# Kernel optimization log

Hardware: AMD Instinct MI355X
Metric: run time of the kernel (lower is better)

## Reference

```python
import jax, jax.numpy as jnp
import numpy as np

B, S, HID = 4, 2048, 2048
NH, NKV, HD = 16, 4, 128  # head_dim = HID // NH
Q_SIZE, KV_SIZE = NH * HD, NKV * HD


def setup_inputs() -> dict:
    key = jax.random.key(0)
    ks = jax.random.split(key, 8)
    pos = jnp.arange(S, dtype=jnp.float32)[:, None]
    inv_freq = 1.0 / (10000.0 ** (jnp.arange(0, HD, 2, dtype=jnp.float32) / HD))  # [HD/2]
    ang = pos * inv_freq[None, :]  # [S, HD/2]
    return {
        "hidden_states": jax.random.normal(ks[0], (B, S, HID), jnp.float32),
        "rotary_pos_emb_cos": jnp.cos(ang),
        "rotary_pos_emb_sin": jnp.sin(ang),
        "w_qkv": jax.random.normal(ks[1], (HID, Q_SIZE + 2 * KV_SIZE), jnp.float32) * (HID ** -0.5),
        "b_qkv": jax.random.normal(ks[2], (Q_SIZE + 2 * KV_SIZE,), jnp.float32) * 0.02,
        "w_o": jax.random.normal(ks[3], (HID, HID), jnp.float32) * (HID ** -0.5),
        "b_o": jax.random.normal(ks[4], (HID,), jnp.float32) * 0.02,
    }


def _apply_rope(x, cos, sin):
    # x: [B, S, H, D]; cos/sin: [S, D/2]; rotate-half (non-interleaved) convention
    d2 = x.shape[-1] // 2
    x1, x2 = x[..., :d2], x[..., d2:]
    c = cos[None, :, None, :]
    s = sin[None, :, None, :]
    return jnp.concatenate([x1 * c - x2 * s, x2 * c + x1 * s], axis=-1)


def reference(hidden_states, rotary_pos_emb_cos, rotary_pos_emb_sin, w_qkv, b_qkv, w_o, b_o):
    b, s, _ = hidden_states.shape
    qkv = hidden_states @ w_qkv + b_qkv  # [B, S, Q_SIZE + 2*KV_SIZE]
    q, k, v = jnp.split(qkv, [Q_SIZE, Q_SIZE + KV_SIZE], axis=-1)
    q = q.reshape(b, s, NH, HD)
    k = k.reshape(b, s, NKV, HD)
    v = v.reshape(b, s, NKV, HD)
    q = _apply_rope(q, rotary_pos_emb_cos, rotary_pos_emb_sin)
    k = _apply_rope(k, rotary_pos_emb_cos, rotary_pos_emb_sin)
    # grouped-query attention: repeat kv heads to match query heads
    g = NH // NKV
    k = jnp.repeat(k, g, axis=2)  # [B, S, NH, HD]
    v = jnp.repeat(v, g, axis=2)
    scale = HD ** -0.5
    scores = jnp.einsum("bshd,bthd->bhst", q, k) * scale  # [B, NH, S, S]
    probs = jax.nn.softmax(scores, axis=-1)
    out = jnp.einsum("bhst,bthd->bshd", probs, v)  # [B, S, NH, HD]
    out = out.reshape(b, s, NH * HD)
    return out @ w_o + b_o
```

## Files before the change

### kernel.cpp

```cpp
#include <hip/hip_runtime.h>
#include <math.h>

#define B_N   4
#define S_N   2048
#define HID_N 2048
#define NH_N  16
#define NKV_N 4
#define HD_N  128
#define QSZ   2048
#define KVSZ  512
#define QKVN  3072
#define M_N   8192

typedef __bf16 bf16;
typedef __bf16 bf16x8 __attribute__((ext_vector_type(8)));
typedef float  f32x4  __attribute__((ext_vector_type(4)));

#define GLL16(gp, lp)                                                          \
  __builtin_amdgcn_global_load_lds(                                            \
      (const __attribute__((address_space(1))) void*)(gp),                     \
      (__attribute__((address_space(3))) void*)(lp), 16, 0, 0)

__device__ __forceinline__ f32x4 mfma16(bf16x8 a, bf16x8 b, f32x4 c) {
  return __builtin_amdgcn_mfma_f32_16x16x32_bf16(a, b, c, 0, 0, 0);
}

__global__ __launch_bounds__(256) void conv_bf16_kernel(
    const float* __restrict__ X, bf16* __restrict__ Y)
{
  size_t i = ((size_t)blockIdx.x * 256 + threadIdx.x) * 8;
  float4 a = *(const float4*)&X[i];
  float4 b = *(const float4*)&X[i + 4];
  union { bf16 h[8]; uint4 u; } pk;
  pk.h[0] = (bf16)a.x; pk.h[1] = (bf16)a.y; pk.h[2] = (bf16)a.z; pk.h[3] = (bf16)a.w;
  pk.h[4] = (bf16)b.x; pk.h[5] = (bf16)b.y; pk.h[6] = (bf16)b.z; pk.h[7] = (bf16)b.w;
  *(uint4*)&Y[i] = pk.u;
}

__global__ __launch_bounds__(256) void convT_kernel(
    const float* __restrict__ W, bf16* __restrict__ Wt, int K, int N)
{
  __shared__ __attribute__((aligned(16))) bf16 tile[64 * 68];
  const int n0 = blockIdx.x * 64, k0 = blockIdx.y * 64;
#pragma unroll
  for (int it = 0; it < 4; ++it) {
    int idx = it * 256 + threadIdx.x;
    int r = idx >> 4, c4 = (idx & 15) << 2;
    float4 v = *(const float4*)&W[(size_t)(k0 + r) * N + n0 + c4];
    union { bf16 h[4]; unsigned long long u; } pk;
    pk.h[0] = (bf16)v.x; pk.h[1] = (bf16)v.y; pk.h[2] = (bf16)v.z; pk.h[3] = (bf16)v.w;
    *(unsigned long long*)&tile[r * 68 + c4] = pk.u;
  }
  __syncthreads();
#pragma unroll
  for (int it = 0; it < 4; ++it) {
    int idx = it * 256 + threadIdx.x;
    int rn = idx >> 4, ck4 = (idx & 15) << 2;
    union { bf16 h[4]; unsigned long long u; } pk;
#pragma unroll
    for (int i = 0; i < 4; ++i) pk.h[i] = tile[(ck4 + i) * 68 + rn];
    *(unsigned long long*)&Wt[(size_t)(n0 + rn) * K + k0 + ck4] = pk.u;
  }
}

template <bool OUT_BF16>
__global__ __launch_bounds__(256, 2) void gemm_bf16_kernel(
    const bf16* __restrict__ A, const bf16* __restrict__ Bt,
    const float* __restrict__ bias, void* __restrict__ Cout,
    int M, int N, int K)
{
  __shared__ __attribute__((aligned(16))) bf16 As[2][128 * 32];
  __shared__ __attribute__((aligned(16))) bf16 Bs[2][128 * 32];

  const int tid  = threadIdx.x;
  const int lane = tid & 63, wv = tid >> 6;
  const int quad = lane >> 4, ln = lane & 15;
  const int row0 = blockIdx.y * 128, col0 = blockIdx.x * 128;
  const int wr = (wv >> 1) * 64, wc = (wv & 1) * 64;

  f32x4 acc[4][4];
  const f32x4 zero = {0.f, 0.f, 0.f, 0.f};
#pragma unroll
  for (int mt = 0; mt < 4; ++mt)
#pragma unroll
    for (int nt = 0; nt < 4; ++nt) acc[mt][nt] = zero;

  const int s0 = wv * 128 + lane;
  const bf16* gA0 = A  + (size_t)(row0 + (s0 >> 2)) * K + (s0 & 3) * 8;
  const bf16* gA1 = gA0 + 16 * (size_t)K;
  const bf16* gB0 = Bt + (size_t)(col0 + (s0 >> 2)) * K + (s0 & 3) * 8;
  const bf16* gB1 = gB0 + 16 * (size_t)K;
  const int lofs0 = wv * 1024, lofs1 = lofs0 + 512;

  GLL16(gA0, &As[0][lofs0]);
  GLL16(gA1, &As[0][lofs1]);
  GLL16(gB0, &Bs[0][lofs0]);
  GLL16(gB1, &Bs[0][lofs1]);
  __syncthreads();

  int cur = 0;
  for (int k0 = 0; k0 < K; k0 += 32, cur ^= 1) {
    const int nk = k0 + 32;
    if (nk < K) {
      GLL16(gA0 + nk, &As[cur ^ 1][lofs0]);
      GLL16(gA1 + nk, &As[cur ^ 1][lofs1]);
      GLL16(gB0 + nk, &Bs[cur ^ 1][lofs0]);
      GLL16(gB1 + nk, &Bs[cur ^ 1][lofs1]);
    }

    bf16x8 a[4], b[4];
#pragma unroll
    for (int mt = 0; mt < 4; ++mt)
      a[mt] = *(const bf16x8*)&As[cur][(wr + mt * 16 + ln) * 32 + quad * 8];
#pragma unroll
    for (int nt = 0; nt < 4; ++nt)
      b[nt] = *(const bf16x8*)&Bs[cur][(wc + nt * 16 + ln) * 32 + quad * 8];
#pragma unroll
    for (int mt = 0; mt < 4; ++mt)
#pragma unroll
      for (int nt = 0; nt < 4; ++nt)
        acc[mt][nt] = mfma16(a[mt], b[nt], acc[mt][nt]);

    __syncthreads();
  }

#pragma unroll
  for (int nt = 0; nt < 4; ++nt) {
    const int c = col0 + wc + nt * 16 + ln;
    const float bv = bias[c];
#pragma unroll
    for (int mt = 0; mt < 4; ++mt) {
#pragma unroll
      for (int r = 0; r < 4; ++r) {
        const int rr = row0 + wr + mt * 16 + quad * 4 + r;
        const float v = acc[mt][nt][r] + bv;
        if (OUT_BF16) ((bf16*)Cout)[(size_t)rr * N + c] = (bf16)v;
        else          ((float*)Cout)[(size_t)rr * N + c] = v;
      }
    }
  }
}

__global__ __launch_bounds__(256) void rope_repack_kernel(
    const bf16* __restrict__ qkvB, const float* __restrict__ cosb,
    const float* __restrict__ sinb, bf16* __restrict__ Qb, bf16* __restrict__ Kb)
{
  int idx = blockIdx.x * 256 + threadIdx.x;
  int j  = idx & 63;
  int m  = (idx >> 6) & (M_N - 1);
  int hh = idx >> 19;
  int b = m >> 11, s = m & (S_N - 1);
  float c  = cosb[s * 64 + j];
  float sn = sinb[s * 64 + j];
  if (hh < NH_N) {
    const bf16* src = qkvB + (size_t)m * QKVN + hh * HD_N;
    float x1 = (float)src[j], x2 = (float)src[j + 64];
    bf16* dst = Qb + ((size_t)(b * NH_N + hh) * S_N + s) * HD_N;
    const float qs = 0.08838834764831845f * 1.4426950408889634f;
    dst[j]      = (bf16)((x1 * c - x2 * sn) * qs);
    dst[j + 64] = (bf16)((x2 * c + x1 * sn) * qs);
  } else {
    int kh = hh - NH_N;
    const bf16* src = qkvB + (size_t)m * QKVN + QSZ + kh * HD_N;
    float x1 = (float)src[j], x2 = (float)src[j + 64];
    bf16* dst = Kb + ((size_t)(b * NKV_N + kh) * S_N + s) * HD_N;
    dst[j]      = (bf16)(x1 * c - x2 * sn);
    dst[j + 64] = (bf16)(x2 * c + x1 * sn);
  }
}

__global__ __launch_bounds__(256) void transposeV_kernel(
    const bf16* __restrict__ qkvB, bf16* __restrict__ Vt)
{
  __shared__ __attribute__((aligned(16))) bf16 tile[64 * 136];
  const int s0 = blockIdx.x * 64;
  const int bkh = blockIdx.y;
  const int b = bkh >> 2, kh = bkh & 3;
#pragma unroll
  for (int it = 0; it < 4; ++it) {
    int ci = it * 256 + threadIdx.x;
    int r = ci >> 4, c = ci & 15;
    uint4 v = *(const uint4*)&qkvB[(size_t)(b * S_N + s0 + r) * QKVN +
                                   QSZ + KVSZ + kh * HD_N + c * 8];
    *(uint4*)&tile[r * 136 + c * 8] = v;
  }
  __syncthreads();
#pragma unroll
  for (int it = 0; it < 4; ++it) {
    int ci = it * 256 + threadIdx.x;
    int d = ci >> 3, c = ci & 7;
    union { bf16 h[8]; uint4 u; } pk;
#pragma unroll
    for (int i = 0; i < 8; ++i) pk.h[i] = tile[(c * 8 + i) * 136 + d];
    *(uint4*)&Vt[((size_t)bkh * HD_N + d) * S_N + s0 + c * 8] = pk.u;
  }
}

__global__ __launch_bounds__(256, 3) void attn_mfma_kernel(
    const bf16* __restrict__ Qb, const bf16* __restrict__ Kb,
    const bf16* __restrict__ Vt, bf16* __restrict__ Ob)
{
  __shared__ __attribute__((aligned(16))) bf16 Ks[2][32 * 128];
  __shared__ __attribute__((aligned(16))) bf16 Vs[2][128 * 32];
  __shared__ __attribute__((aligned(16))) bf16 Ps[128 * 40];

  const int tid  = threadIdx.x;
  const int lane = tid & 63, wv = tid >> 6;
  const int quad = lane >> 4, ln = lane & 15;

  const int gid = blockIdx.x;
  const int xcd = gid & 7, sl = gid >> 3;
  const int grp = xcd * 2 + (sl >> 6);
  const int within = sl & 63;
  const int b = grp >> 2, kh = grp & 3;
  const int h = kh * 4 + (within >> 4);
  const int q0 = (within & 15) * 128;

  const bf16* Qg = Qb + ((size_t)(b * NH_N + h) * S_N + q0) * HD_N;
  const bf16* Kg = Kb + (size_t)(b * NKV_N + kh) * S_N * HD_N;
  const bf16* Vg = Vt + (size_t)(b * NKV_N + kh) * HD_N * S_N;

  bf16x8 aq[2][4];
#pragma unroll
  for (int g = 0; g < 2; ++g) {
    const bf16* qrow = Qg + (size_t)((wv * 2 + g) * 16 + ln) * HD_N;
#pragma unroll
    for (int dc = 0; dc < 4; ++dc)
      aq[g][dc] = *(const bf16x8*)&qrow[(dc * 4 + quad) * 8];
  }

  const bf16* kga[2];
  const bf16* vga[2];
#pragma unroll
  for (int t = 0; t < 2; ++t) {
    int slot = (t * 4 + wv) * 64 + lane;
    int row = slot >> 4, cc = slot & 15;
    int csrc = (cc & 8) | ((cc & 7) ^ (row & 7));
    kga[t] = Kg + (size_t)row * 128 + csrc * 8;
    int dv = slot >> 2, ccv = slot & 3;
    int csv = ccv ^ ((dv >> 1) & 3);
    vga[t] = Vg + (size_t)dv * S_N + csv * 8;
  }

#pragma unroll
  for (int t = 0; t < 2; ++t) GLL16(kga[t], &Ks[0][(t * 4 + wv) * 512]);
#pragma unroll
  for (int t = 0; t < 2; ++t) GLL16(vga[t], &Vs[0][(t * 4 + wv) * 512]);

  bf16x8 bones;
#pragma unroll
  for (int j = 0; j < 8; ++j) bones[j] = (ln == 0) ? (bf16)1.0f : (bf16)0.0f;

  f32x4 accO[2][8];
  const f32x4 zero = {0.f, 0.f, 0.f, 0.f};
#pragma unroll
  for (int g = 0; g < 2; ++g)
#pragma unroll
    for (int dt = 0; dt < 8; ++dt) accO[g][dt] = zero;
  f32x4 accL[2] = {zero, zero};

  __syncthreads();

  int cur = 0;
  for (int kt = 0; kt < S_N; kt += 32, cur ^= 1) {
    const int nkt = kt + 32;
    if (nkt < S_N) {
#pragma unroll
      for (int t = 0; t < 2; ++t)
        GLL16(kga[t] + (size_t)nkt * 128, &Ks[cur ^ 1][(t * 4 + wv) * 512]);
#pragma unroll
      for (int t = 0; t < 2; ++t)
        GLL16(vga[t] + nkt, &Vs[cur ^ 1][(t * 4 + wv) * 512]);
    }
    const bf16* Kc = Ks[cur];
    const bf16* Vc = Vs[cur];

    f32x4 accS[2][2];
#pragma unroll
    for (int g = 0; g < 2; ++g)
#pragma unroll
      for (int nt = 0; nt < 2; ++nt) accS[g][nt] = zero;
#pragma unroll
    for (int nt = 0; nt < 2; ++nt) {
      const int kp = nt * 16 + ln;
#pragma unroll
      for (int dc = 0; dc < 4; ++dc) {
        int c = dc * 4 + quad;
        int cs = (c & 8) | ((c & 7) ^ (kp & 7));
        bf16x8 bk = *(const bf16x8*)&Kc[kp * 128 + cs * 8];
        accS[0][nt] = mfma16(aq[0][dc], bk, accS[0][nt]);
        accS[1][nt] = mfma16(aq[1][dc], bk, accS[1][nt]);
      }
    }

#pragma unroll
    for (int g = 0; g < 2; ++g)
#pragma unroll
      for (int r = 0; r < 4; ++r) {
        const int q = (wv * 2 + g) * 16 + quad * 4 + r;
        bf16* pr = &Ps[q * 40 + ln];
        pr[0]  = (bf16)__builtin_amdgcn_exp2f(accS[g][0][r]);
        pr[16] = (bf16)__builtin_amdgcn_exp2f(accS[g][1][r]);
      }

    bf16x8 ap[2];
#pragma unroll
    for (int g = 0; g < 2; ++g) {
      ap[g] = *(const bf16x8*)&Ps[((wv * 2 + g) * 16 + ln) * 40 + quad * 8];
      accL[g] = mfma16(ap[g], bones, accL[g]);
    }
#pragma unroll
    for (int dt = 0; dt < 8; ++dt) {
      const int d = dt * 16 + ln;
      int cs = quad ^ ((d >> 1) & 3);
      bf16x8 bv = *(const bf16x8*)&Vc[d * 32 + cs * 8];
      accO[0][dt] = mfma16(ap[0], bv, accO[0][dt]);
      accO[1][dt] = mfma16(ap[1], bv, accO[1][dt]);
    }

    __syncthreads();
  }

#pragma unroll
  for (int g = 0; g < 2; ++g)
#pragma unroll
    for (int r = 0; r < 4; ++r) {
      const float l = __shfl(accL[g][r], lane & 48);
      const float inv = 1.f / l;
      const int q = q0 + (wv * 2 + g) * 16 + quad * 4 + r;
      const size_t base = ((size_t)b * S_N + q) * HID_N + h * HD_N;
#pragma unroll
      for (int dt = 0; dt < 8; ++dt)
        Ob[base + dt * 16 + ln] = (bf16)(accO[g][dt][r] * inv);
    }
}

extern "C" void kernel_launch(void* const* d_in, const int* in_sizes, int n_in,
                              void* d_out, int out_size, void* d_ws, size_t ws_size,
                              hipStream_t stream) {
  const float* hidden = (const float*)d_in[0];
  const float* cosb   = (const float*)d_in[1];
  const float* sinb   = (const float*)d_in[2];
  const float* w_qkv  = (const float*)d_in[3];
  const float* b_qkv  = (const float*)d_in[4];
  const float* w_o    = (const float*)d_in[5];
  const float* b_o    = (const float*)d_in[6];
  float* out = (float*)d_out;

  char* w = (char*)d_ws;
  bf16* qkvB  = (bf16*)(w);
  bf16* Qb    = (bf16*)(w + 50331648);
  bf16* Kb    = (bf16*)(w + 83886080);
  bf16* Vt    = (bf16*)(w + 92274688);
  bf16* wqkvT = (bf16*)(w + 100663296);
  bf16* woT   = (bf16*)(w + 113246208);
  bf16* hidB  = (bf16*)(w + 121634816);
  bf16* attnB = hidB;

  conv_bf16_kernel<<<(M_N * HID_N) / (256 * 8), 256, 0, stream>>>(hidden, hidB);
  convT_kernel<<<dim3(QKVN / 64, HID_N / 64), 256, 0, stream>>>(w_qkv, wqkvT, HID_N, QKVN);
  convT_kernel<<<dim3(HID_N / 64, HID_N / 64), 256, 0, stream>>>(w_o, woT, HID_N, HID_N);

  gemm_bf16_kernel<true><<<dim3(QKVN / 128, M_N / 128), 256, 0, stream>>>(
      hidB, wqkvT, b_qkv, qkvB, M_N, QKVN, HID_N);

  rope_repack_kernel<<<(M_N * (NH_N + NKV_N) * 64) / 256, 256, 0, stream>>>(
      qkvB, cosb, sinb, Qb, Kb);
  transposeV_kernel<<<dim3(S_N / 64, B_N * NKV_N), 256, 0, stream>>>(qkvB, Vt);

  attn_mfma_kernel<<<1024, 256, 0, stream>>>(Qb, Kb, Vt, attnB);

  gemm_bf16_kernel<false><<<dim3(HID_N / 128, M_N / 128), 256, 0, stream>>>(
      attnB, woT, b_o, out, M_N, HID_N, HID_N);
}
```

Measured before the change: 544.6 us.

## Replace GEMMs with 256x256-tile 8-wave pipelined kernel and XCD-aware block mapping

Both projection GEMMs now run on a 512-thread kernel that computes 256x256 output tiles with a K-step of 64. The K-step is split into four phases, and LDS staging for future tiles is interleaved with the MFMA work using explicit vmcnt waits, raw barriers and s_setprio. Block IDs are remapped so neighbouring tiles land on the same XCD. Larger tiles raise data reuse and the deeper pipeline hides load latency, at the cost of more registers and LDS (128 KB), fewer blocks (384 and 256), and hand-tuned waitcnt logic that could be fragile.

```diff
diff --git a/kernel.cpp b/kernel.cpp
--- a/kernel.cpp
+++ b/kernel.cpp
@@ -21,6 +21,9 @@
       (const __attribute__((address_space(1))) void*)(gp),                     \
       (__attribute__((address_space(3))) void*)(lp), 16, 0, 0)
 
+#define CFENCE asm volatile("" ::: "memory")
+#define BARRIER do { CFENCE; __builtin_amdgcn_s_barrier(); CFENCE; } while (0)
+
 __device__ __forceinline__ f32x4 mfma16(bf16x8 a, bf16x8 b, f32x4 c) {
   return __builtin_amdgcn_mfma_f32_16x16x32_bf16(a, b, c, 0, 0, 0);
 }
@@ -64,76 +67,103 @@
 }
 
 template <bool OUT_BF16>
-__global__ __launch_bounds__(256, 2) void gemm_bf16_kernel(
+__global__ __launch_bounds__(512, 2) void gemm256_kernel(
     const bf16* __restrict__ A, const bf16* __restrict__ Bt,
     const float* __restrict__ bias, void* __restrict__ Cout,
-    int M, int N, int K)
-{
-  __shared__ __attribute__((aligned(16))) bf16 As[2][128 * 32];
-  __shared__ __attribute__((aligned(16))) bf16 Bs[2][128 * 32];
+    int M, int N, int K, int nbx)
+{
+  __shared__ __attribute__((aligned(16))) bf16 Asl[2][2][256 * 32];
+  __shared__ __attribute__((aligned(16))) bf16 Bsl[2][2][256 * 32];
 
   const int tid  = threadIdx.x;
   const int lane = tid & 63, wv = tid >> 6;
   const int quad = lane >> 4, ln = lane & 15;
-  const int row0 = blockIdx.y * 128, col0 = blockIdx.x * 128;
-  const int wr = (wv >> 1) * 64, wc = (wv & 1) * 64;
-
-  f32x4 acc[4][4];
+  const int wm = wv >> 2, wn = wv & 3;
+
+  const int cpx = (int)gridDim.x >> 3;
+  const int gid = ((int)blockIdx.x & 7) * cpx + ((int)blockIdx.x >> 3);
+  const int row0 = (gid / nbx) * 256, col0 = (gid % nbx) * 256;
+
+  const int slot0 = (wv * 2 + 0) * 64 + lane;
+  const int slot1 = (wv * 2 + 1) * 64 + lane;
+  const bf16* gA0 = A  + (size_t)(row0 + (slot0 >> 2)) * K + (slot0 & 3) * 8;
+  const bf16* gA1 = A  + (size_t)(row0 + (slot1 >> 2)) * K + (slot1 & 3) * 8;
+  const bf16* gB0 = Bt + (size_t)(col0 + (slot0 >> 2)) * K + (slot0 & 3) * 8;
+  const bf16* gB1 = Bt + (size_t)(col0 + (slot1 >> 2)) * K + (slot1 & 3) * 8;
+  const int lu0 = (wv * 2 + 0) * 512, lu1 = (wv * 2 + 1) * 512;
+
+#define STG_A(buf, kh, t) do {                                               \
+    GLL16(gA0 + (size_t)(t) * 64 + (kh) * 32, &Asl[buf][kh][lu0]);           \
+    GLL16(gA1 + (size_t)(t) * 64 + (kh) * 32, &Asl[buf][kh][lu1]);           \
+  } while (0)
+#define STG_B(buf, kh, t) do {                                               \
+    GLL16(gB0 + (size_t)(t) * 64 + (kh) * 32, &Bsl[buf][kh][lu0]);           \
+    GLL16(gB1 + (size_t)(t) * 64 + (kh) * 32, &Bsl[buf][kh][lu1]);           \
+  } while (0)
+
+  f32x4 acc[8][4];
   const f32x4 zero = {0.f, 0.f, 0.f, 0.f};
 #pragma unroll
-  for (int mt = 0; mt < 4; ++mt)
-#pragma unroll
-    for (int nt = 0; nt < 4; ++nt) acc[mt][nt] = zero;
-
-  const int s0 = wv * 128 + lane;
-  const bf16* gA0 = A  + (size_t)(row0 + (s0 >> 2)) * K + (s0 & 3) * 8;
-  const bf16* gA1 = gA0 + 16 * (size_t)K;
-  const bf16* gB0 = Bt + (size_t)(col0 + (s0 >> 2)) * K + (s0 & 3) * 8;
-  const bf16* gB1 = gB0 + 16 * (size_t)K;
-  const int lofs0 = wv * 1024, lofs1 = lofs0 + 512;
-
-  GLL16(gA0, &As[0][lofs0]);
-  GLL16(gA1, &As[0][lofs1]);
-  GLL16(gB0, &Bs[0][lofs0]);
-  GLL16(gB1, &Bs[0][lofs1]);
-  __syncthreads();
+  for (int mf = 0; mf < 8; ++mf)
+#pragma unroll
+    for (int nf = 0; nf < 4; ++nf) acc[mf][nf] = zero;
+
+  bf16x8 a[4], bfr[2][4];
+  const int NT = K >> 6;
+
+  STG_B(0, 0, 0); STG_B(0, 1, 0); STG_A(0, 0, 0); STG_A(0, 1, 0);
+  STG_B(1, 0, 1); STG_B(1, 1, 1); STG_A(1, 0, 1);
+  CFENCE; asm volatile("s_waitcnt vmcnt(6)" ::: "memory");
+  BARRIER;
+
+#define PH(mh, kh, READ_B, STAGE_STMT, WAIT_STMT) do {                       \
+    const bf16* Ab = &Asl[cur][kh][(wm * 128 + (mh) * 64 + ln) * 32 + quad * 8]; \
+    _Pragma("unroll")                                                        \
+    for (int mf = 0; mf < 4; ++mf)                                           \
+      a[mf] = *(const bf16x8*)(Ab + mf * 16 * 32);                           \
+    if (READ_B) {                                                            \
+      const bf16* Bb = &Bsl[cur][kh][(wn * 64 + ln) * 32 + quad * 8];        \
+      _Pragma("unroll")                                                      \
+      for (int nf = 0; nf < 4; ++nf)                                         \
+        bfr[kh][nf] = *(const bf16x8*)(Bb + nf * 16 * 32);                   \
+    }                                                                        \
+    STAGE_STMT;                                                              \
+    BARRIER;                                                                 \
+    __builtin_amdgcn_s_setprio(1);                                           \
+    _Pragma("unroll")                                                        \
+    for (int mf = 0; mf < 4; ++mf)                                           \
+      _Pragma("unroll")                                                      \
+      for (int nf = 0; nf < 4; ++nf)                                         \
+        acc[(mh) * 4 + mf][nf] = mfma16(a[mf], bfr[kh][nf],                  \
+                                        acc[(mh) * 4 + mf][nf]);             \
+    __builtin_amdgcn_s_setprio(0);                                           \
+    WAIT_STMT;                                                               \
+    BARRIER;                                                                 \
+  } while (0)
 
   int cur = 0;
-  for (int k0 = 0; k0 < K; k0 += 32, cur ^= 1) {
-    const int nk = k0 + 32;
-    if (nk < K) {
-      GLL16(gA0 + nk, &As[cur ^ 1][lofs0]);
-      GLL16(gA1 + nk, &As[cur ^ 1][lofs1]);
-      GLL16(gB0 + nk, &Bs[cur ^ 1][lofs0]);
-      GLL16(gB1 + nk, &Bs[cur ^ 1][lofs1]);
-    }
-
-    bf16x8 a[4], b[4];
-#pragma unroll
-    for (int mt = 0; mt < 4; ++mt)
-      a[mt] = *(const bf16x8*)&As[cur][(wr + mt * 16 + ln) * 32 + quad * 8];
-#pragma unroll
-    for (int nt = 0; nt < 4; ++nt)
-      b[nt] = *(const bf16x8*)&Bs[cur][(wc + nt * 16 + ln) * 32 + quad * 8];
-#pragma unroll
-    for (int mt = 0; mt < 4; ++mt)
-#pragma unroll
-      for (int nt = 0; nt < 4; ++nt)
-        acc[mt][nt] = mfma16(a[mt], b[nt], acc[mt][nt]);
-
-    __syncthreads();
-  }
-
-#pragma unroll
-  for (int nt = 0; nt < 4; ++nt) {
-    const int c = col0 + wc + nt * 16 + ln;
+  for (int t = 0; t < NT; ++t, cur ^= 1) {
+    PH(0, 0, 1, { if (t + 1 < NT) STG_A(cur ^ 1, 1, t + 1); }, {});
+    PH(0, 1, 1, { if (t + 2 < NT) STG_B(cur, 0, t + 2); },     {});
+    PH(1, 0, 0, { if (t + 2 < NT) STG_B(cur, 1, t + 2); },     {});
+    PH(1, 1, 0, { if (t + 2 < NT) STG_A(cur, 0, t + 2); },
+       { if (t == NT - 2) { asm volatile("s_waitcnt vmcnt(0)" ::: "memory"); } \
+         else if (t < NT - 2) { asm volatile("s_waitcnt vmcnt(6)" ::: "memory"); } });
+  }
+#undef PH
+#undef STG_A
+#undef STG_B
+
+#pragma unroll
+  for (int nf = 0; nf < 4; ++nf) {
+    const int c = col0 + wn * 64 + nf * 16 + ln;
     const float bv = bias[c];
 #pragma unroll
-    for (int mt = 0; mt < 4; ++mt) {
+    for (int mf = 0; mf < 8; ++mf) {
 #pragma unroll
       for (int r = 0; r < 4; ++r) {
-        const int rr = row0 + wr + mt * 16 + quad * 4 + r;
-        const float v = acc[mt][nt][r] + bv;
+        const int rr = row0 + wm * 128 + mf * 16 + quad * 4 + r;
+        const float v = acc[mf][nf][r] + bv;
         if (OUT_BF16) ((bf16*)Cout)[(size_t)rr * N + c] = (bf16)v;
         else          ((float*)Cout)[(size_t)rr * N + c] = v;
       }
@@ -361,8 +391,8 @@
   convT_kernel<<<dim3(QKVN / 64, HID_N / 64), 256, 0, stream>>>(w_qkv, wqkvT, HID_N, QKVN);
   convT_kernel<<<dim3(HID_N / 64, HID_N / 64), 256, 0, stream>>>(w_o, woT, HID_N, HID_N);
 
-  gemm_bf16_kernel<true><<<dim3(QKVN / 128, M_N / 128), 256, 0, stream>>>(
-      hidB, wqkvT, b_qkv, qkvB, M_N, QKVN, HID_N);
+  gemm256_kernel<true><<<(M_N / 256) * (QKVN / 256), 512, 0, stream>>>(
+      hidB, wqkvT, b_qkv, qkvB, M_N, QKVN, HID_N, QKVN / 256);
 
   rope_repack_kernel<<<(M_N * (NH_N + NKV_N) * 64) / 256, 256, 0, stream>>>(
       qkvB, cosb, sinb, Qb, Kb);
@@ -370,6 +400,6 @@
 
   attn_mfma_kernel<<<1024, 256, 0, stream>>>(Qb, Kb, Vt, attnB);
 
-  gemm_bf16_kernel<false><<<dim3(HID_N / 128, M_N / 128), 256, 0, stream>>>(
-      attnB, woT, b_o, out, M_N, HID_N, HID_N);
-}
+  gemm256_kernel<false><<<(M_N / 256) * (HID_N / 256), 512, 0, stream>>>(
+      attnB, woT, b_o, out, M_N, HID_N, HID_N, HID_N / 256);
+}
```

Result: no change. 554.2 us (+1.8%).
